# Performance work log

Hardware: AMD Instinct MI355X
Metric: run time of the kernel (lower is better)

Reference implementation:

```python
import jax, jax.numpy as jnp
import numpy as np

B, N, C = 128, 512, 512  # batch, num_proposals, hidden_dim
K = 3                    # kernel_size
EPS = 1e-5               # LayerNorm eps (torch default)


def setup_inputs() -> dict:
    key = jax.random.key(0)
    k1, k2, k3, k4 = jax.random.split(key, 4)
    query = jax.random.normal(k1, (B, N, C), dtype=jnp.float32)
    value = jax.random.normal(k2, (B, N, C), dtype=jnp.float32)
    # nn.Linear(C, N+K): store transposed weight [C, N+K] for x @ W
    lim = 1.0 / np.sqrt(C)
    W_lin = jax.random.uniform(k3, (C, N + K), minval=-lim, maxval=lim, dtype=jnp.float32)
    b_lin = jax.random.uniform(k4, (N + K,), minval=-lim, maxval=lim, dtype=jnp.float32)
    gamma = jnp.ones((C,), dtype=jnp.float32)
    beta = jnp.zeros((C,), dtype=jnp.float32)
    return {"query": query, "value": value, "W_lin": W_lin, "b_lin": b_lin,
            "gamma": gamma, "beta": beta}


def reference(query, value, W_lin, b_lin, gamma, beta):
    # dynamic weights: [B, N, N+K]
    dy = jnp.einsum('bnc,ck->bnk', query, W_lin) + b_lin
    dw = dy[..., :K]          # depthwise kernel  [B, N, 3]
    pw = dy[..., K:]          # pointwise weights [B, N(out), N(in)]
    # depthwise conv1d along C, groups=N, padding='same' (cross-correlation)
    vp = jnp.pad(value, ((0, 0), (0, 0), (1, 1)))
    depth = (dw[..., 0:1] * vp[..., 0:C]
             + dw[..., 1:2] * vp[..., 1:C + 1]
             + dw[..., 2:3] * vp[..., 2:C + 2])
    depth = jax.nn.relu(depth)
    # pointwise (1x1) conv across proposals: out[b,m,c] = sum_n pw[b,m,n] * depth[b,n,c]
    out = jnp.einsum('bmn,bnc->bmc', pw, depth)
    # LayerNorm over last dim C
    mu = jnp.mean(out, axis=-1, keepdims=True)
    var = jnp.mean(jnp.square(out - mu), axis=-1, keepdims=True)
    return (out - mu) * jax.lax.rsqrt(var + EPS) * gamma + beta
```

## Files before the change

### kernel.cpp

```cpp
#include <hip/hip_runtime.h>
#include <hip/hip_bf16.h>

typedef unsigned short u16;
typedef unsigned int u32;
typedef __attribute__((ext_vector_type(8))) short short8;
typedef __attribute__((ext_vector_type(8))) unsigned short ushort8;
typedef __attribute__((ext_vector_type(4))) float f32x4;

#define AS1 __attribute__((address_space(1)))
#define AS3 __attribute__((address_space(3)))

#define Bb_ 128
#define Nn_ 512
#define Cc_ 512
#define NK_ 515

__device__ __forceinline__ u16 f2bf(float f) {
    union { float f; u32 i; } t; t.f = f;
    u32 x = t.i;
    u32 r = (x + 0x7fffu + ((x >> 16) & 1u)) >> 16;
    return (u16)r;
}

#define ROWS_PER_WAVE 32
__global__ void prep_kernel(const float* __restrict__ q, const float* __restrict__ W,
                            const float* __restrict__ bl,
                            u16* __restrict__ qbf, float* __restrict__ dw) {
    __shared__ float wc[3][512];
    int tid = threadIdx.x;
    for (int idx = tid; idx < 3 * 512; idx += 256) {
        int j = idx >> 9, c = idx & 511;
        wc[j][c] = W[c * NK_ + j];
    }
    __syncthreads();

    int w = tid >> 6, l = tid & 63;
    int c0 = l * 8;
    float w0[8], w1[8], w2[8];
#pragma unroll
    for (int e = 0; e < 8; e++) {
        w0[e] = wc[0][c0 + e];
        w1[e] = wc[1][c0 + e];
        w2[e] = wc[2][c0 + e];
    }
    float bl0 = bl[0], bl1 = bl[1], bl2 = bl[2];

    size_t row0 = (size_t)blockIdx.x * (4 * ROWS_PER_WAVE) + (size_t)w * ROWS_PER_WAVE;
#pragma unroll 2
    for (int rr = 0; rr < ROWS_PER_WAVE; rr++) {
        size_t row = row0 + rr;
        const float* qr = q + row * Cc_;
        f32x4 x0 = *(const f32x4*)(qr + c0);
        f32x4 x1 = *(const f32x4*)(qr + c0 + 4);
        float xf[8] = {x0[0], x0[1], x0[2], x0[3], x1[0], x1[1], x1[2], x1[3]};
        ushort8 y;
        float s0 = 0.f, s1 = 0.f, s2 = 0.f;
#pragma unroll
        for (int e = 0; e < 8; e++) {
            float qf = xf[e];
            y[e] = f2bf(qf);
            s0 += qf * w0[e];
            s1 += qf * w1[e];
            s2 += qf * w2[e];
        }
        *(ushort8*)(qbf + row * Cc_ + c0) = y;
#pragma unroll
        for (int off = 32; off > 0; off >>= 1) {
            s0 += __shfl_xor(s0, off);
            s1 += __shfl_xor(s1, off);
            s2 += __shfl_xor(s2, off);
        }
        if (l == 0) {
            dw[row * 3 + 0] = s0 + bl0;
            dw[row * 3 + 1] = s1 + bl1;
            dw[row * 3 + 2] = s2 + bl2;
        }
    }
}

__global__ void wt_kernel(const float* __restrict__ W, u16* __restrict__ WT) {
    int n = blockIdx.y;
    int c = blockIdx.x * 256 + threadIdx.x;
    WT[n * Cc_ + c] = f2bf(W[c * NK_ + n + 3]);
}

__global__ void depthT_kernel(const float* __restrict__ val, const float* __restrict__ dw,
                              u16* __restrict__ dT) {
    __shared__ float vt[64][67];
    __shared__ float dws[64][3];
    int b = blockIdx.z;
    int c0 = blockIdx.x * 64;
    int n0 = blockIdx.y * 64;
    int tid = threadIdx.x;

    const float* vbase = val + ((size_t)b * Nn_ + n0) * Cc_;
    for (int idx = tid; idx < 64 * 66; idx += 256) {
        int r = idx / 66, cc = idx % 66;
        int c = c0 - 1 + cc;
        float x = 0.f;
        if (c >= 0 && c < Cc_) x = vbase[(size_t)r * Cc_ + c];
        vt[r][cc] = x;
    }
    if (tid < 192) {
        int r = tid / 3, j = tid % 3;
        dws[r][j] = dw[((size_t)b * Nn_ + n0 + r) * 3 + j];
    }
    __syncthreads();

    int nn = tid & 63;
    int ccb = tid >> 6;
    u16* out = dT + ((size_t)b * Cc_ + c0) * Nn_ + n0;
    float d0 = dws[nn][0], d1 = dws[nn][1], d2 = dws[nn][2];
#pragma unroll
    for (int p = 0; p < 16; p++) {
        int cc = ccb + p * 4;
        float x = d0 * vt[nn][cc] + d1 * vt[nn][cc + 1] + d2 * vt[nn][cc + 2];
        x = x > 0.f ? x : 0.f;
        out[(size_t)cc * Nn_ + nn] = f2bf(x);
    }
}

template <int LN>
__global__ __launch_bounds__(512, 2) void gemm_k(const u16* __restrict__ A,
                                                 const u16* __restrict__ Bt,
                                                 void* __restrict__ Outv,
                                                 const float* __restrict__ bias,
                                                 const float* __restrict__ gamma,
                                                 const float* __restrict__ beta,
                                                 long strideB) {
    __shared__ __align__(16) u16 lA[2][128 * 32];
    __shared__ __align__(16) u16 lB[2][512 * 32];

    int wg = blockIdx.x;
    int xcd = wg & 7, slot = wg >> 3;
    int b = xcd * 16 + (slot >> 2);
    int tm = slot & 3;

    const u16* Ab = A + ((size_t)b * Nn_ + (size_t)tm * 128) * 512;
    const u16* Bb = Bt + (size_t)b * strideB;

    int tid = threadIdx.x, w = tid >> 6, l = tid & 63;
    int rsub = l >> 2, csub = l & 3;
    int row_l = l & 15, quad = l >> 4;
    int n_off = w * 64;

    f32x4 acc[8][4];
#pragma unroll
    for (int i = 0; i < 8; i++)
#pragma unroll
        for (int j = 0; j < 4; j++) acc[i][j] = (f32x4){0.f, 0.f, 0.f, 0.f};

    auto STAGE = [&](int buf, int kt) {
        int kof = kt * 32;
#pragma unroll
        for (int j = 0; j < 4; j++) {
            int seg = w * 4 + j;
            int r = seg * 16 + rsub;
            const u16* gB = Bb + (size_t)r * 512 + kof + csub * 8;
            __builtin_amdgcn_global_load_lds((const AS1 u32*)gB,
                                             (AS3 u32*)&lB[buf][seg * 512], 16, 0, 0);
        }
        {
            int r = w * 16 + rsub;
            const u16* gA = Ab + (size_t)r * 512 + kof + csub * 8;
            __builtin_amdgcn_global_load_lds((const AS1 u32*)gA,
                                             (AS3 u32*)&lA[buf][w * 512], 16, 0, 0);
        }
    };

    STAGE(0, 0);
    __syncthreads();
    int cur = 0;
    for (int kt = 0; kt < 16; kt++) {
        if (kt < 15) STAGE(cur ^ 1, kt + 1);

        short8 aF[8], bF[4];
#pragma unroll
        for (int i = 0; i < 8; i++)
            aF[i] = *(const short8*)&lA[cur][(i * 16 + row_l) * 32 + quad * 8];
#pragma unroll
        for (int j = 0; j < 4; j++)
            bF[j] = *(const short8*)&lB[cur][(n_off + j * 16 + row_l) * 32 + quad * 8];

#pragma unroll
        for (int i = 0; i < 8; i++)
#pragma unroll
            for (int j = 0; j < 4; j++)
                acc[i][j] = __builtin_amdgcn_mfma_f32_16x16x32_bf16(aF[i], bF[j], acc[i][j], 0, 0, 0);

        __syncthreads();
        cur ^= 1;
    }

    if (!LN) {
        u16* outb = (u16*)Outv + ((size_t)b * Nn_ + (size_t)tm * 128) * 512;
#pragma unroll
        for (int j = 0; j < 4; j++) {
            int gn = n_off + j * 16 + row_l;
            float bv = bias[gn];
#pragma unroll
            for (int i = 0; i < 8; i++) {
#pragma unroll
                for (int r = 0; r < 4; r++) {
                    int gm = i * 16 + quad * 4 + r;
                    outb[(size_t)gm * 512 + gn] = f2bf(acc[i][j][r] + bv);
                }
            }
        }
    } else {
        float* red  = (float*)&lA[0][0];
        float* musd = (float*)&lB[0][0];

#pragma unroll
        for (int i = 0; i < 8; i++) {
#pragma unroll
            for (int r = 0; r < 4; r++) {
                float a0 = acc[i][0][r], a1 = acc[i][1][r], a2 = acc[i][2][r], a3 = acc[i][3][r];
                float s  = a0 + a1 + a2 + a3;
                float ss = a0 * a0 + a1 * a1 + a2 * a2 + a3 * a3;
#pragma unroll
                for (int off = 8; off > 0; off >>= 1) {
                    s  += __shfl_xor(s, off);
                    ss += __shfl_xor(ss, off);
                }
                if (row_l == 0) {
                    int row = i * 16 + quad * 4 + r;
                    red[(w * 128 + row) * 2 + 0] = s;
                    red[(w * 128 + row) * 2 + 1] = ss;
                }
            }
        }
        __syncthreads();
        if (tid < 128) {
            float s = 0.f, ss = 0.f;
#pragma unroll
            for (int ww = 0; ww < 8; ww++) {
                s  += red[(ww * 128 + tid) * 2 + 0];
                ss += red[(ww * 128 + tid) * 2 + 1];
            }
            float mu = s * (1.f / 512.f);
            float var = ss * (1.f / 512.f) - mu * mu;
            musd[tid] = mu;
            musd[128 + tid] = rsqrtf(var + 1e-5f);
        }
        __syncthreads();

        float* outb = (float*)Outv + ((size_t)b * Nn_ + (size_t)tm * 128) * 512;
        int gc0 = n_off + row_l;
        float gv[4], bv[4];
#pragma unroll
        for (int j = 0; j < 4; j++) {
            gv[j] = gamma[gc0 + j * 16];
            bv[j] = beta[gc0 + j * 16];
        }
#pragma unroll
        for (int i = 0; i < 8; i++) {
#pragma unroll
            for (int r = 0; r < 4; r++) {
                int row = i * 16 + quad * 4 + r;
                float mu = musd[row], rs = musd[128 + row];
#pragma unroll
                for (int j = 0; j < 4; j++)
                    outb[(size_t)row * 512 + gc0 + j * 16] = (acc[i][j][r] - mu) * rs * gv[j] + bv[j];
            }
        }
    }
}

extern "C" void kernel_launch(void* const* d_in, const int* in_sizes, int n_in,
                              void* d_out, int out_size, void* d_ws, size_t ws_size,
                              hipStream_t stream) {
    const float* q     = (const float*)d_in[0];
    const float* v     = (const float*)d_in[1];
    const float* W     = (const float*)d_in[2];
    const float* bl    = (const float*)d_in[3];
    const float* gamma = (const float*)d_in[4];
    const float* beta  = (const float*)d_in[5];

    char* ws = (char*)d_ws;
    u16*   WT  = (u16*)ws;
    float* dw  = (float*)(ws + 524288);
    u16*   pw  = (u16*)(ws + 1310720);
    u16*   dT  = (u16*)(ws + 68419584);
    float* out = (float*)d_out;
    u16*   qbf = (u16*)d_out;

    prep_kernel<<<dim3((Bb_ * Nn_) / (4 * ROWS_PER_WAVE)), 256, 0, stream>>>(q, W, bl, qbf, dw);
    wt_kernel<<<dim3(2, 512), 256, 0, stream>>>(W, WT);
    depthT_kernel<<<dim3(8, 8, Bb_), 256, 0, stream>>>(v, dw, dT);

    gemm_k<0><<<dim3(512), 512, 0, stream>>>(qbf, WT, pw, bl + 3, nullptr, nullptr, 0L);
    gemm_k<1><<<dim3(512), 512, 0, stream>>>(pw, dT, out, nullptr, gamma, beta,
                                             (long)Cc_ * Nn_);
}
```

Baseline: 513.9 us.

## Triple-buffer GEMM LDS pipeline and vectorize depthwise conv stores

The GEMM main loop moves from double to triple buffering. Loads are issued two K-steps ahead, and each step uses explicit vmcnt waits with a single barrier instead of two __syncthreads per iteration, to hide global-to-LDS latency. The depthwise+ReLU kernel now has each thread compute 8 consecutive proposals and write them as one 16-byte ushort8 store instead of scattered 2-byte stores. The trade-off is LDS use rising to about 120KB per block, which likely stops two blocks sharing a CU despite launch_bounds(512,2).

```diff
diff --git a/kernel.cpp b/kernel.cpp
--- a/kernel.cpp
+++ b/kernel.cpp
@@ -107,16 +107,27 @@
     }
     __syncthreads();
 
-    int nn = tid & 63;
-    int ccb = tid >> 6;
+    int nn0 = (tid & 7) * 8;
+    int ccx = tid >> 3;
+    float d0[8], d1[8], d2[8];
+#pragma unroll
+    for (int e = 0; e < 8; e++) {
+        d0[e] = dws[nn0 + e][0];
+        d1[e] = dws[nn0 + e][1];
+        d2[e] = dws[nn0 + e][2];
+    }
     u16* out = dT + ((size_t)b * Cc_ + c0) * Nn_ + n0;
-    float d0 = dws[nn][0], d1 = dws[nn][1], d2 = dws[nn][2];
-#pragma unroll
-    for (int p = 0; p < 16; p++) {
-        int cc = ccb + p * 4;
-        float x = d0 * vt[nn][cc] + d1 * vt[nn][cc + 1] + d2 * vt[nn][cc + 2];
-        x = x > 0.f ? x : 0.f;
-        out[(size_t)cc * Nn_ + nn] = f2bf(x);
+#pragma unroll
+    for (int h = 0; h < 2; h++) {
+        int cc = ccx + h * 32;
+        ushort8 y;
+#pragma unroll
+        for (int e = 0; e < 8; e++) {
+            float x = d0[e] * vt[nn0 + e][cc] + d1[e] * vt[nn0 + e][cc + 1] +
+                      d2[e] * vt[nn0 + e][cc + 2];
+            y[e] = f2bf(x > 0.f ? x : 0.f);
+        }
+        *(ushort8*)(out + (size_t)cc * Nn_ + nn0) = y;
     }
 }
 
@@ -128,8 +139,8 @@
                                                  const float* __restrict__ gamma,
                                                  const float* __restrict__ beta,
                                                  long strideB) {
-    __shared__ __align__(16) u16 lA[2][128 * 32];
-    __shared__ __align__(16) u16 lB[2][512 * 32];
+    __shared__ __align__(16) u16 lA[3][128 * 32];
+    __shared__ __align__(16) u16 lB[3][512 * 32];
 
     int wg = blockIdx.x;
     int xcd = wg & 7, slot = wg >> 3;
@@ -169,11 +180,20 @@
     };
 
     STAGE(0, 0);
-    __syncthreads();
-    int cur = 0;
+    STAGE(1, 1);
     for (int kt = 0; kt < 16; kt++) {
-        if (kt < 15) STAGE(cur ^ 1, kt + 1);
-
+        if (kt < 15) asm volatile("s_waitcnt vmcnt(5)" ::: "memory");
+        else         asm volatile("s_waitcnt vmcnt(0)" ::: "memory");
+        __builtin_amdgcn_s_barrier();
+        __builtin_amdgcn_sched_barrier(0);
+
+        if (kt < 14) {
+            int sb = kt + 2;
+            STAGE(sb - (sb >= 3 ? 3 : 0) - (sb >= 6 ? 3 : 0) - (sb >= 9 ? 3 : 0) -
+                      (sb >= 12 ? 3 : 0) - (sb >= 15 ? 3 : 0), sb);
+        }
+
+        int cur = kt % 3;
         short8 aF[8], bF[4];
 #pragma unroll
         for (int i = 0; i < 8; i++)
@@ -187,10 +207,8 @@
 #pragma unroll
             for (int j = 0; j < 4; j++)
                 acc[i][j] = __builtin_amdgcn_mfma_f32_16x16x32_bf16(aF[i], bF[j], acc[i][j], 0, 0, 0);
-
-        __syncthreads();
-        cur ^= 1;
-    }
+    }
+    __syncthreads();
 
     if (!LN) {
         u16* outb = (u16*)Outv + ((size_t)b * Nn_ + (size_t)tm * 128) * 512;
```

After: 503.8 us. -2.0%, faster.
